# Kernel optimization log

Measured on AMD Instinct MI355X. Metric: run time of the kernel, lower is better.

## Reference

```python
import jax, jax.numpy as jnp
import numpy as np
import math

N = 100000      # nodes
E = 1600000     # edges
D = 128         # in_channels
C = 256         # number of dominant-set cliques
HID = 64        # mlp_hidden
RATIO = 0.8
K = int(math.ceil(RATIO * N))  # 80000 topk nodes per view


def setup_inputs() -> dict:
    key = jax.random.key(0)
    ks = jax.random.split(key, 18)
    s = 0.05
    return {
        "x": jax.random.normal(ks[0], (N, D), jnp.float32),
        "edge_index": jax.random.randint(ks[1], (2, E), 0, N, dtype=jnp.int32),
        "batch": jnp.zeros((N,), jnp.int32),
        "cluster_id": jax.random.randint(ks[2], (N,), 0, C, dtype=jnp.int32),
        # MLP scorer: Linear(D,HID) -> ReLU -> Linear(HID,1)
        "mlp_w1": jax.random.normal(ks[3], (D, HID), jnp.float32) * s,
        "mlp_b1": jnp.zeros((HID,), jnp.float32),
        "mlp_w2": jax.random.normal(ks[4], (HID, 1), jnp.float32) * s,
        "mlp_b2": jnp.zeros((1,), jnp.float32),
        # GATConv(D, 1, heads=1)
        "gat_w": jax.random.normal(ks[5], (D, 1), jnp.float32) * s,
        "gat_a_src": jax.random.normal(ks[6], (1,), jnp.float32) * s,
        "gat_a_dst": jax.random.normal(ks[7], (1,), jnp.float32) * s,
        "gat_b": jnp.zeros((1,), jnp.float32),
        # InterChannelGCN attention Linear(2D,1) split into fine/coarse halves
        "att_w_fine": jax.random.normal(ks[8], (D,), jnp.float32) * s,
        "att_w_coarse": jax.random.normal(ks[9], (D,), jnp.float32) * s,
        "att_b": jnp.zeros((1,), jnp.float32),
        # InterChannelGCN transform Linear(D,D)
        "trans_w": jax.random.normal(ks[10], (D, D), jnp.float32) * s,
        "trans_b": jnp.zeros((D,), jnp.float32),
    }


def _inter_channel_gcn(h_fine, H_coarse, R, wa, wb, ab, tw, tb):
    # attention(Linear(2D,1)) on concat(h_fine_i, H_coarse_j) == h_fine@wa + H_coarse@wb + b
    scores = h_fine @ wa[:, None] + (H_coarse @ wb)[None, :] + ab[0]   # [K, C]
    attn = jax.nn.softmax(scores * R, axis=-1)                          # mask-by-multiply, as original
    out = attn @ H_coarse + h_fine                                      # add_self=True
    return jax.nn.relu(out @ tw + tb)                                   # normalize=False


def reference(x, edge_index, batch, cluster_id,
              mlp_w1, mlp_b1, mlp_w2, mlp_b2,
              gat_w, gat_a_src, gat_a_dst, gat_b,
              att_w_fine, att_w_coarse, att_b, trans_w, trans_b):
    src, dst = edge_index[0], edge_index[1]

    # --- DominantClustering('avg'): cluster means as coarse features ---
    counts = jax.ops.segment_sum(jnp.ones((N,), jnp.float32), cluster_id, num_segments=C)
    Hcoarse = jax.ops.segment_sum(x, cluster_id, num_segments=C) / jnp.maximum(counts, 1.0)[:, None]

    # --- feature view: MLP score + topk ---
    feature_score = (jax.nn.relu(x @ mlp_w1 + mlp_b1) @ mlp_w2 + mlp_b2)[:, 0]   # [N]
    _, feat_idx = jax.lax.top_k(feature_score, K)
    feature_view3 = x[feat_idx]
    R_feat = jax.nn.one_hot(cluster_id[feat_idx], C, dtype=x.dtype)              # relationship matrix
    fuse1 = _inter_channel_gcn(feature_view3, Hcoarse, R_feat,
                               att_w_fine, att_w_coarse, att_b, trans_w, trans_b)

    # --- local view: GATConv(D,1,heads=1) score + topk ---
    h = x @ gat_w                                                                 # [N,1]
    e = jax.nn.leaky_relu(gat_a_src[0] * h[src, 0] + gat_a_dst[0] * h[dst, 0], 0.2)  # [E]
    m = jax.ops.segment_max(e, dst, num_segments=N)
    ex = jnp.exp(e - m[dst])
    den = jax.ops.segment_sum(ex, dst, num_segments=N)
    alpha = ex / jnp.maximum(den[dst], 1e-16)
    localview_score = jax.ops.segment_sum(alpha * h[src, 0], dst, num_segments=N) + gat_b[0]
    _, local_idx = jax.lax.top_k(localview_score, K)
    local_view1 = x[local_idx]
    R_local = jax.nn.one_hot(cluster_id[local_idx], C, dtype=x.dtype)
    fuse2 = _inter_channel_gcn(local_view1, Hcoarse, R_local,
                               att_w_fine, att_w_coarse, att_b, trans_w, trans_b)

    # --- union, edge filtering + remapping (padded fixed shapes) ---
    in_feat = jnp.zeros((N,), bool).at[feat_idx].set(True)
    in_local = jnp.zeros((N,), bool).at[local_idx].set(True)
    union = in_feat | in_local
    mapping = jnp.where(union, jnp.cumsum(union.astype(jnp.int32)) - 1, -1)
    m0, m1 = mapping[src], mapping[dst]
    valid = (m0 >= 0) & (m1 >= 0)
    edge_index_topk = jnp.where(valid[None, :], jnp.stack([m0, m1]), -1)          # [2,E], -1 = dropped

    # --- fused features (faithful to original's fuse1/fuse2 index swap) ---
    A = jnp.zeros((N, D), x.dtype).at[feat_idx].set(fuse2)    # fuse2 indexed by feature topk position
    B = jnp.zeros((N, D), x.dtype).at[local_idx].set(fuse1)   # fuse1 indexed by local topk position
    both = in_feat & in_local
    Fp = jnp.where(both[:, None], (A + B) * 0.5, A + B)
    Fp = jnp.where(union[:, None], Fp, 0.0)                   # [N,D], zero outside union

    new_batch = jnp.where(union, batch, -1)
    return Fp, edge_index_topk, new_batch
```

## Files before the change

kernel.cpp:

```cpp
#include <hip/hip_runtime.h>
#include <hip/hip_bf16.h>
#include <stdint.h>

#define N 100000
#define E_ 1600000
#define D 128
#define C_ 256
#define HID 64
#define KSEL 80000
#define NB 4096
#define CHUNK 1024
#define NCHUNK ((N + CHUNK - 1) / CHUNK)
#define CSEG 32
#define NBK 782
#define BCAP 2560
#define RMAX 2048

__device__ __forceinline__ unsigned enc_f(float f) {
  unsigned b = __float_as_uint(f);
  return (b & 0x80000000u) ? ~b : (b | 0x80000000u);
}
__device__ __forceinline__ float dec_f(unsigned u) {
  unsigned b = (u & 0x80000000u) ? (u ^ 0x80000000u) : ~u;
  return __uint_as_float(b);
}

__global__ __launch_bounds__(256) void k_hist_cluster(const int* __restrict__ cid, int* __restrict__ ccount) {
  int n = blockIdx.x * 256 + threadIdx.x;
  if (n < N) atomicAdd(&ccount[cid[n]], 1);
}

__global__ __launch_bounds__(1024) void k_scan_small(const int* __restrict__ in0, int* __restrict__ out0, int n) {
  __shared__ int sums[1024];
  const int* in = in0 + (size_t)blockIdx.x * n;
  int* out = out0 + (size_t)blockIdx.x * n;
  int t = threadIdx.x;
  int per = (n + 1023) / 1024;
  int base = t * per;
  int loc = 0;
  for (int k = 0; k < per; ++k) { int i = base + k; if (i < n) loc += in[i]; }
  sums[t] = loc; __syncthreads();
  for (int off = 1; off < 1024; off <<= 1) {
    int v = (t >= off) ? sums[t - off] : 0;
    __syncthreads();
    sums[t] += v;
    __syncthreads();
  }
  int run = (t == 0) ? 0 : sums[t - 1];
  for (int k = 0; k < per; ++k) { int i = base + k; if (i < n) { out[i] = run; run += in[i]; } }
}

__global__ __launch_bounds__(256) void k_scatter_cluster(const int* __restrict__ cid, const int* __restrict__ cstart,
                                                         int* __restrict__ ccur, int* __restrict__ cslot) {
  int n = blockIdx.x * 256 + threadIdx.x;
  if (n < N) {
    int c = cid[n];
    int p = cstart[c] + atomicAdd(&ccur[c], 1);
    cslot[p] = n;
  }
}

__global__ __launch_bounds__(128) void k_cluster_partial(const float* __restrict__ x, const int* __restrict__ cstart,
                                                         const int* __restrict__ ccount, const int* __restrict__ cslot,
                                                         float* __restrict__ Hc) {
  int c = blockIdx.x >> 5;
  int s = blockIdx.x & (CSEG - 1);
  int d = threadIdx.x;
  int st = cstart[c], cnt = ccount[c];
  int seg = (cnt + CSEG - 1) / CSEG;
  int lo = s * seg;
  int hi = min(cnt, lo + seg);
  if (lo >= hi) return;
  float acc = 0.f;
  int k = lo;
  for (; k + 2 <= hi; k += 2) {
    int n0 = cslot[st + k], n1 = cslot[st + k + 1];
    float v0 = x[(size_t)n0 * D + d];
    float v1 = x[(size_t)n1 * D + d];
    acc += v0 + v1;
  }
  if (k < hi) acc += x[(size_t)cslot[st + k] * D + d];
  atomicAdd(&Hc[(size_t)c * D + d], acc);
}

__global__ __launch_bounds__(128) void k_mean_gdot(const int* __restrict__ ccount, const float* __restrict__ wb,
                                                   float* __restrict__ Hc, float* __restrict__ gdot) {
  __shared__ float red[128];
  int c = blockIdx.x, d = threadIdx.x;
  float hv = Hc[(size_t)c * D + d] / (float)max(ccount[c], 1);
  Hc[(size_t)c * D + d] = hv;
  red[d] = hv * wb[d];
  __syncthreads();
  if (d < 64) {
    float v = red[d] + red[d + 64];
    for (int off = 32; off; off >>= 1) v += __shfl_down(v, off);
    if (d == 0) gdot[c] = v;
  }
}

__global__ __launch_bounds__(128) void k_S_SW_HW(const float* __restrict__ Hc, const float* __restrict__ tw,
                                                 float* __restrict__ SW, float* __restrict__ HW) {
  __shared__ float Sl[128];
  int b = blockIdx.x, t = threadIdx.x;
  if (b == 0) {
    float s = 0.f;
    for (int c = 0; c < C_; ++c) s += Hc[(size_t)c * D + t];
    Sl[t] = s;
    __syncthreads();
    float acc = 0.f;
    for (int d = 0; d < D; ++d) acc = fmaf(Sl[d], tw[(size_t)d * D + t], acc);
    SW[t] = acc;
  } else {
    const float* src = Hc + (size_t)(b - 1) * D;
    float acc = 0.f;
    for (int d = 0; d < D; ++d) acc = fmaf(src[d], tw[(size_t)d * D + t], acc);
    HW[(size_t)(b - 1) * D + t] = acc;
  }
}

__global__ __launch_bounds__(256, 4) void k_score64(const float* __restrict__ x, const float* __restrict__ w1,
                                                    const float* __restrict__ b1, const float* __restrict__ w2,
                                                    const float* __restrict__ b2, const float* __restrict__ gw,
                                                    const float* __restrict__ wa, float* __restrict__ scoreF,
                                                    float* __restrict__ hg, float* __restrict__ aDot) {
  __shared__ float xld[64 * D];
  int tid = threadIdx.x;
  int base = blockIdx.x * 64;
#pragma unroll
  for (int k = 0; k < 8; ++k) {
    int i = k * 256 + tid;
    int r = i >> 5, off = i & 31;
    int n = base + r;
    float4 v = make_float4(0.f, 0.f, 0.f, 0.f);
    if (n < N) v = ((const float4*)(x + (size_t)n * D))[off];
    ((float4*)xld)[i] = v;
  }
  __syncthreads();

  int rg = tid >> 5;
  int cg = tid & 31;
  int c2 = cg * 2;
  float acc[8][2] = {};
  const float* xb = xld + rg * 8 * D;
  for (int d4 = 0; d4 < D; d4 += 4) {
    float2 wv0 = *(const float2*)(w1 + (size_t)(d4 + 0) * HID + c2);
    float2 wv1 = *(const float2*)(w1 + (size_t)(d4 + 1) * HID + c2);
    float2 wv2 = *(const float2*)(w1 + (size_t)(d4 + 2) * HID + c2);
    float2 wv3 = *(const float2*)(w1 + (size_t)(d4 + 3) * HID + c2);
#pragma unroll
    for (int r = 0; r < 8; ++r) {
      float4 xv = *(const float4*)(xb + r * D + d4);
      acc[r][0] = fmaf(xv.x, wv0.x, acc[r][0]);
      acc[r][1] = fmaf(xv.x, wv0.y, acc[r][1]);
      acc[r][0] = fmaf(xv.y, wv1.x, acc[r][0]);
      acc[r][1] = fmaf(xv.y, wv1.y, acc[r][1]);
      acc[r][0] = fmaf(xv.z, wv2.x, acc[r][0]);
      acc[r][1] = fmaf(xv.z, wv2.y, acc[r][1]);
      acc[r][0] = fmaf(xv.w, wv3.x, acc[r][0]);
      acc[r][1] = fmaf(xv.w, wv3.y, acc[r][1]);
    }
  }
  float2 b1v = *(const float2*)(b1 + c2);
  float2 w2v = *(const float2*)(w2 + c2);
  float bb = b2[0];
#pragma unroll
  for (int r = 0; r < 8; ++r) {
    float p = fmaxf(acc[r][0] + b1v.x, 0.f) * w2v.x + fmaxf(acc[r][1] + b1v.y, 0.f) * w2v.y;
#pragma unroll
    for (int off = 16; off; off >>= 1) p += __shfl_xor(p, off);
    if (cg == 0) {
      int n = base + rg * 8 + r;
      if (n < N) scoreF[n] = p + bb;
    }
  }
  float4 gwv = *(const float4*)(gw + cg * 4);
  float4 wav = *(const float4*)(wa + cg * 4);
#pragma unroll
  for (int r = 0; r < 8; ++r) {
    int row = rg * 8 + r;
    float4 xv = *(const float4*)(xld + row * D + cg * 4);
    float hp = xv.x * gwv.x + xv.y * gwv.y + xv.z * gwv.z + xv.w * gwv.w;
    float ap = xv.x * wav.x + xv.y * wav.y + xv.z * wav.z + xv.w * wav.w;
#pragma unroll
    for (int off = 16; off; off >>= 1) {
      hp += __shfl_xor(hp, off);
      ap += __shfl_xor(ap, off);
    }
    if (cg == 0) {
      int n = base + row;
      if (n < N) { hg[n] = hp; aDot[n] = ap; }
    }
  }
}

__global__ __launch_bounds__(1024) void k_escatter(const int* __restrict__ ei, const float* __restrict__ hg,
                                                   const float* __restrict__ asrc, const float* __restrict__ adst,
                                                   int* __restrict__ gcnt, uint2* __restrict__ payload) {
  __shared__ int lcnt[NBK];
  __shared__ int lbase[NBK];
  int tid = threadIdx.x;
  for (int i = tid; i < NBK; i += 1024) lcnt[i] = 0;
  int e0 = blockIdx.x * 8192;
  int es[8], ed[8];
#pragma unroll
  for (int k = 0; k < 8; ++k) {
    int e = e0 + k * 1024 + tid;
    bool v = (e < E_);
    es[k] = v ? ei[e] : -1;
    ed[k] = v ? ei[E_ + e] : -1;
  }
  __syncthreads();
#pragma unroll
  for (int k = 0; k < 8; ++k)
    if (ed[k] >= 0) atomicAdd(&lcnt[ed[k] >> 7], 1);
  __syncthreads();
  for (int i = tid; i < NBK; i += 1024) {
    int c = lcnt[i];
    lbase[i] = c ? atomicAdd(&gcnt[i], c) : 0;
    lcnt[i] = 0;
  }
  __syncthreads();
  float as = asrc[0], ad = adst[0];
#pragma unroll
  for (int k = 0; k < 8; ++k) {
    if (ed[k] < 0) continue;
    int s = es[k], d = ed[k];
    int b = d >> 7, dl = d & 127;
    float z = as * hg[s] + ad * hg[d];
    float ev = (z > 0.f) ? z : 0.2f * z;
    int pos = lbase[b] + atomicAdd(&lcnt[b], 1);
    if (pos < BCAP) {
      uint2 rec;
      rec.x = __float_as_uint(ev);
      rec.y = (unsigned)s | ((unsigned)dl << 24);
      payload[(size_t)b * BCAP + pos] = rec;
    }
  }
}

__global__ __launch_bounds__(256) void k_esoftmax(const uint2* __restrict__ payload, const int* __restrict__ gcnt,
                                                  const float* __restrict__ hg, const float* __restrict__ gb,
                                                  float* __restrict__ scoreL) {
  __shared__ unsigned mS[128];
  __shared__ float dS[128];
  __shared__ float nS[128];
  int b = blockIdx.x;
  int tid = threadIdx.x;
  if (tid < 128) { mS[tid] = 0u; dS[tid] = 0.f; nS[tid] = 0.f; }
  __syncthreads();
  int cnt = min(gcnt[b], BCAP);
  const uint2* bp = payload + (size_t)b * BCAP;
  for (int i = tid; i < cnt; i += 256) {
    uint2 r = bp[i];
    atomicMax(&mS[r.y >> 24], enc_f(__uint_as_float(r.x)));
  }
  __syncthreads();
  for (int i = tid; i < cnt; i += 256) {
    uint2 r = bp[i];
    int d = r.y >> 24;
    float ex = expf(__uint_as_float(r.x) - dec_f(mS[d]));
    atomicAdd(&dS[d], ex);
  }
  __syncthreads();
  for (int i = tid; i < cnt; i += 256) {
    uint2 r = bp[i];
    int d = r.y >> 24;
    float ex = expf(__uint_as_float(r.x) - dec_f(mS[d]));
    float alpha = ex / fmaxf(dS[d], 1e-16f);
    float h = hg[r.y & 0xFFFFFFu];
    atomicAdd(&nS[d], alpha * h);
  }
  __syncthreads();
  if (tid < 128) {
    int dst = b * 128 + tid;
    if (dst < N) scoreL[dst] = nS[tid] + gb[0];
  }
}

__global__ __launch_bounds__(256) void k_minmax2(const float* __restrict__ sc2, unsigned* __restrict__ mm) {
  __shared__ unsigned smx[256], smn[256];
  int v = blockIdx.y;
  const float* sc = sc2 + (size_t)v * N;
  int t = threadIdx.x; int n = blockIdx.x * 256 + t;
  unsigned val = (n < N) ? enc_f(sc[n]) : 0u;
  smx[t] = (n < N) ? val : 0u;
  smn[t] = (n < N) ? val : 0xFFFFFFFFu;
  __syncthreads();
  for (int off = 128; off; off >>= 1) {
    if (t < off) {
      smx[t] = max(smx[t], smx[t + off]);
      smn[t] = min(smn[t], smn[t + off]);
    }
    __syncthreads();
  }
  if (t == 0) { atomicMax(&mm[v], smx[0]); atomicMin(&mm[2 + v], smn[0]); }
}

__global__ __launch_bounds__(256) void k_bucket_hist2(const float* __restrict__ sc2, const unsigned* __restrict__ mm,
                                                      int* __restrict__ bucket2, int* __restrict__ hist2) {
  int v = blockIdx.y;
  int n = blockIdx.x * 256 + threadIdx.x;
  if (n >= N) return;
  const float* sc = sc2 + (size_t)v * N;
  float smax = dec_f(mm[v]), smin = dec_f(mm[2 + v]);
  float range = smax - smin;
  float scale = (range > 0.f) ? ((float)NB / range) : 0.f;
  float t = (smax - sc[n]) * scale;
  int b = (int)t;
  b = b < 0 ? 0 : (b > NB - 1 ? NB - 1 : b);
  bucket2[(size_t)v * N + n] = b;
  atomicAdd(&hist2[v * NB + b], 1);
}

__global__ __launch_bounds__(256) void k_bucket_scatter2(const int* __restrict__ bucket2, const int* __restrict__ start2,
                                                         int* __restrict__ cur2, int* __restrict__ slot2) {
  int v = blockIdx.y;
  int n = blockIdx.x * 256 + threadIdx.x;
  if (n >= N) return;
  int b = bucket2[(size_t)v * N + n];
  slot2[(size_t)v * N + start2[v * NB + b] + atomicAdd(&cur2[v * NB + b], 1)] = n;
}

__global__ __launch_bounds__(64) void k_bucket_rank3(const float* __restrict__ sc2, const int* __restrict__ start2,
                                                     const int* __restrict__ hist2, const int* __restrict__ slot2,
                                                     int* __restrict__ rank2, int* __restrict__ sorted2) {
  __shared__ unsigned long long keys[RMAX];
  int v = blockIdx.y;
  int b = blockIdx.x;
  int st = start2[v * NB + b], cnt = hist2[v * NB + b];
  if (cnt == 0) return;
  const float* sc = sc2 + (size_t)v * N;
  const int* slot = slot2 + (size_t)v * N;
  int* rank = rank2 + (size_t)v * N;
  int* sorted = sorted2 + (size_t)v * N;
  int tid = threadIdx.x;
  if (cnt <= RMAX) {
    for (int i = tid; i < cnt; i += 64) {
      int m = slot[st + i];
      keys[i] = (((unsigned long long)(~enc_f(sc[m]))) << 32) | (unsigned)m;
    }
    __syncthreads();
    for (int i = tid; i < cnt; i += 64) {
      unsigned long long mykey = keys[i];
      int r = 0;
      for (int j = 0; j < cnt; ++j) r += (keys[j] < mykey) ? 1 : 0;
      int m = (int)(mykey & 0xFFFFFFFFu);
      rank[m] = st + r;
      sorted[st + r] = m;
    }
  } else {
    for (int i = tid; i < cnt; i += 64) {
      int m = slot[st + i];
      unsigned long long mykey = (((unsigned long long)(~enc_f(sc[m]))) << 32) | (unsigned)m;
      int r = 0;
      for (int j = 0; j < cnt; ++j) {
        int mj = slot[st + j];
        unsigned long long k = (((unsigned long long)(~enc_f(sc[mj]))) << 32) | (unsigned)mj;
        r += (k < mykey) ? 1 : 0;
      }
      rank[m] = st + r;
      sorted[st + r] = m;
    }
  }
}

__global__ __launch_bounds__(1024) void k_union_chunksum(const int* __restrict__ rankF, const int* __restrict__ rankL,
                                                         int* __restrict__ csum) {
  __shared__ int red[1024];
  int t = threadIdx.x; int i = blockIdx.x * 1024 + t;
  int u = (i < N) ? (((rankF[i] < KSEL) || (rankL[i] < KSEL)) ? 1 : 0) : 0;
  red[t] = u; __syncthreads();
  for (int off = 512; off; off >>= 1) { if (t < off) red[t] += red[t + off]; __syncthreads(); }
  if (t == 0) csum[blockIdx.x] = red[0];
}

__global__ __launch_bounds__(1024) void k_union_map(const int* __restrict__ rankF, const int* __restrict__ rankL,
                                                    const int* __restrict__ cstart, const int* __restrict__ batch,
                                                    int* __restrict__ mapping, float* __restrict__ outBatch) {
  __shared__ int sums[1024];
  int t = threadIdx.x; int i = blockIdx.x * 1024 + t;
  int u = (i < N) ? (((rankF[i] < KSEL) || (rankL[i] < KSEL)) ? 1 : 0) : 0;
  sums[t] = u; __syncthreads();
  for (int off = 1; off < 1024; off <<= 1) {
    int v = (t >= off) ? sums[t - off] : 0;
    __syncthreads();
    sums[t] += v;
    __syncthreads();
  }
  if (i < N) {
    mapping[i] = u ? (cstart[blockIdx.x] + sums[t] - 1) : -1;
    outBatch[i] = u ? (float)batch[i] : -1.0f;
  }
}

__global__ __launch_bounds__(256) void k_edge_out(const int* __restrict__ ei, const int* __restrict__ mapping,
                                                  float* __restrict__ outE) {
  int e = blockIdx.x * 256 + threadIdx.x;
  if (e >= E_) return;
  int m0 = mapping[ei[e]], m1 = mapping[ei[E_ + e]];
  bool valid = (m0 >= 0) && (m1 >= 0);
  outE[e] = valid ? (float)m0 : -1.f;
  outE[E_ + e] = valid ? (float)m1 : -1.f;
}

__global__ __launch_bounds__(256) void k_zero_rows(const int* __restrict__ mapping, float* __restrict__ Fp) {
  int i = blockIdx.x * 256 + threadIdx.x;
  int n = i >> 5;
  if (n < N && mapping[n] < 0) ((float4*)Fp)[i] = make_float4(0.f, 0.f, 0.f, 0.f);
}

__global__ __launch_bounds__(256, 4) void k_fuse64(const float* __restrict__ x, const float* __restrict__ tw,
                                                   const float* __restrict__ tb, const float* __restrict__ SW,
                                                   const float* __restrict__ HW, const float* __restrict__ gdot,
                                                   const float* __restrict__ aDot, const int* __restrict__ cid,
                                                   const int* __restrict__ srcL, const int* __restrict__ tgtL,
                                                   const float* __restrict__ attb, const int* __restrict__ rankF,
                                                   float* __restrict__ Fp, int accum) {
  __shared__ float xld[64 * D];
  __shared__ float pq[64 * 2];
  __shared__ int mt[64 * 2];
  __shared__ int ft[64];
  int tid = threadIdx.x;
  int base = blockIdx.x * 64;
  if (tid < 64) {
    int ws = srcL[base + tid];
    int cc = cid[ws];
    int tg = tgtL[base + tid];
    mt[tid * 2] = cc;
    mt[tid * 2 + 1] = tg;
    ft[tid] = (rankF[tg] < KSEL) ? 1 : 0;
    float s = aDot[ws] + gdot[cc] + attb[0];
    float mx = fmaxf(s, 0.f);
    float esm = expf(s - mx), eom = expf(-mx);
    float dn = esm + 255.f * eom;
    pq[tid * 2] = esm / dn;
    pq[tid * 2 + 1] = eom / dn;
  }
#pragma unroll
  for (int k = 0; k < 8; ++k) {
    int i = k * 256 + tid;
    int r = i >> 5, off = i & 31;
    int ws = srcL[base + r];
    ((float4*)xld)[i] = ((const float4*)(x + (size_t)ws * D))[off];
  }
  __syncthreads();

  int rg = tid >> 5;
  int c4 = (tid & 31) * 4;
  float acc[8][4] = {};
  const float* xb = xld + rg * 8 * D;
  float4 t0 = *(const float4*)(tw + (size_t)0 * D + c4);
  float4 t1 = *(const float4*)(tw + (size_t)1 * D + c4);
  float4 t2 = *(const float4*)(tw + (size_t)2 * D + c4);
  float4 t3 = *(const float4*)(tw + (size_t)3 * D + c4);
  for (int d4 = 0; d4 < D; d4 += 4) {
    float4 u0, u1, u2, u3;
    if (d4 + 4 < D) {
      u0 = *(const float4*)(tw + (size_t)(d4 + 4) * D + c4);
      u1 = *(const float4*)(tw + (size_t)(d4 + 5) * D + c4);
      u2 = *(const float4*)(tw + (size_t)(d4 + 6) * D + c4);
      u3 = *(const float4*)(tw + (size_t)(d4 + 7) * D + c4);
    } else {
      u0 = u1 = u2 = u3 = make_float4(0.f, 0.f, 0.f, 0.f);
    }
#pragma unroll
    for (int r = 0; r < 8; ++r) {
      float4 xv = *(const float4*)(xb + r * D + d4);
      acc[r][0] = fmaf(xv.x, t0.x, acc[r][0]);
      acc[r][1] = fmaf(xv.x, t0.y, acc[r][1]);
      acc[r][2] = fmaf(xv.x, t0.z, acc[r][2]);
      acc[r][3] = fmaf(xv.x, t0.w, acc[r][3]);
      acc[r][0] = fmaf(xv.y, t1.x, acc[r][0]);
      acc[r][1] = fmaf(xv.y, t1.y, acc[r][1]);
      acc[r][2] = fmaf(xv.y, t1.z, acc[r][2]);
      acc[r][3] = fmaf(xv.y, t1.w, acc[r][3]);
      acc[r][0] = fmaf(xv.z, t2.x, acc[r][0]);
      acc[r][1] = fmaf(xv.z, t2.y, acc[r][1]);
      acc[r][2] = fmaf(xv.z, t2.z, acc[r][2]);
      acc[r][3] = fmaf(xv.z, t2.w, acc[r][3]);
      acc[r][0] = fmaf(xv.w, t3.x, acc[r][0]);
      acc[r][1] = fmaf(xv.w, t3.y, acc[r][1]);
      acc[r][2] = fmaf(xv.w, t3.z, acc[r][2]);
      acc[r][3] = fmaf(xv.w, t3.w, acc[r][3]);
    }
    t0 = u0; t1 = u1; t2 = u2; t3 = u3;
  }

  float4 tbv = *(const float4*)(tb + c4);
  float4 swv = *(const float4*)(SW + c4);
#pragma unroll
  for (int r = 0; r < 8; ++r) {
    int row = rg * 8 + r;
    float p = pq[row * 2], q = pq[row * 2 + 1];
    int cc = mt[row * 2];
    int tgt = mt[row * 2 + 1];
    float4 hw = *(const float4*)(HW + (size_t)cc * D + c4);
    float4 o;
    o.x = fmaxf(acc[r][0] + tbv.x + q * swv.x + (p - q) * hw.x, 0.f);
    o.y = fmaxf(acc[r][1] + tbv.y + q * swv.y + (p - q) * hw.y, 0.f);
    o.z = fmaxf(acc[r][2] + tbv.z + q * swv.z + (p - q) * hw.z, 0.f);
    o.w = fmaxf(acc[r][3] + tbv.w + q * swv.w + (p - q) * hw.w, 0.f);
    float4* dst = (float4*)(Fp + (size_t)tgt * D + c4);
    if (accum && ft[row]) {
      float4 old = *dst;
      o.x = (o.x + old.x) * 0.5f;
      o.y = (o.y + old.y) * 0.5f;
      o.z = (o.z + old.z) * 0.5f;
      o.w = (o.w + old.w) * 0.5f;
    }
    *dst = o;
  }
}

extern "C" void kernel_launch(void* const* d_in, const int* in_sizes, int n_in,
                              void* d_out, int out_size, void* d_ws, size_t ws_size,
                              hipStream_t stream) {
  const float* x   = (const float*)d_in[0];
  const int* ei    = (const int*)d_in[1];
  const int* batch = (const int*)d_in[2];
  const int* cid   = (const int*)d_in[3];
  const float* w1  = (const float*)d_in[4];
  const float* b1  = (const float*)d_in[5];
  const float* w2  = (const float*)d_in[6];
  const float* b2  = (const float*)d_in[7];
  const float* gw  = (const float*)d_in[8];
  const float* gas = (const float*)d_in[9];
  const float* gad = (const float*)d_in[10];
  const float* gb  = (const float*)d_in[11];
  const float* wa  = (const float*)d_in[12];
  const float* wb  = (const float*)d_in[13];
  const float* ab  = (const float*)d_in[14];
  const float* tw  = (const float*)d_in[15];
  const float* tb  = (const float*)d_in[16];
  (void)in_sizes; (void)n_in; (void)ws_size; (void)out_size;

  char* p = (char*)d_ws;
  auto alloc = [&](size_t bytes) -> char* {
    char* r = p;
    p += (bytes + 255) & ~(size_t)255;
    return r;
  };
  int* ccount    = (int*)alloc(C_ * 4);
  int* ccur      = (int*)alloc(C_ * 4);
  unsigned* mm   = (unsigned*)alloc(16);
  int* hist2     = (int*)alloc(2 * NB * 4);
  int* cur2      = (int*)alloc(2 * NB * 4);
  float* Hc      = (float*)alloc((size_t)C_ * D * 4);
  int* gcnt      = (int*)alloc(NBK * 4);
  size_t zeroBytes = (size_t)(p - (char*)d_ws);
  int* cstart   = (int*)alloc(C_ * 4);
  int* cslot    = (int*)alloc((size_t)N * 4);
  float* gdot   = (float*)alloc(C_ * 4);
  float* SW     = (float*)alloc(D * 4);
  float* HW     = (float*)alloc((size_t)C_ * D * 4);
  float* score2 = (float*)alloc((size_t)2 * N * 4);
  float* hg     = (float*)alloc((size_t)N * 4);
  float* aDot   = (float*)alloc((size_t)N * 4);
  uint2* payload = (uint2*)alloc((size_t)NBK * BCAP * 8);
  int* bucket2  = (int*)alloc((size_t)2 * N * 4);
  int* start2   = (int*)alloc(2 * NB * 4);
  int* slot2    = (int*)alloc((size_t)2 * N * 4);
  int* sorted2  = (int*)alloc((size_t)2 * N * 4);
  int* rank2    = (int*)alloc((size_t)2 * N * 4);
  int* csums    = (int*)alloc(NCHUNK * 4);
  int* cstarts  = (int*)alloc(NCHUNK * 4);
  int* mapping  = (int*)alloc((size_t)N * 4);

  float* scoreF = score2;
  float* scoreL = score2 + N;
  int* sortedF  = sorted2;
  int* sortedL  = sorted2 + N;
  int* rankF    = rank2;
  int* rankL    = rank2 + N;

  float* outF = (float*)d_out;
  float* outE = outF + (size_t)N * D;
  float* outB = outE + (size_t)2 * E_;

  hipMemsetAsync(d_ws, 0, zeroBytes, stream);
  hipMemsetAsync(mm + 2, 0xFF, 8, stream);

  k_hist_cluster<<<(N + 255) / 256, 256, 0, stream>>>(cid, ccount);
  k_scan_small<<<1, 1024, 0, stream>>>(ccount, cstart, C_);
  k_scatter_cluster<<<(N + 255) / 256, 256, 0, stream>>>(cid, cstart, ccur, cslot);
  k_cluster_partial<<<C_ * CSEG, 128, 0, stream>>>(x, cstart, ccount, cslot, Hc);
  k_mean_gdot<<<C_, 128, 0, stream>>>(ccount, wb, Hc, gdot);
  k_S_SW_HW<<<C_ + 1, 128, 0, stream>>>(Hc, tw, SW, HW);

  k_score64<<<(N + 63) / 64, 256, 0, stream>>>(x, w1, b1, w2, b2, gw, wa, scoreF, hg, aDot);
  k_escatter<<<(E_ + 8191) / 8192, 1024, 0, stream>>>(ei, hg, gas, gad, gcnt, payload);
  k_esoftmax<<<NBK, 256, 0, stream>>>(payload, gcnt, hg, gb, scoreL);

  dim3 g2((N + 255) / 256, 2);
  k_minmax2<<<g2, 256, 0, stream>>>(score2, mm);
  k_bucket_hist2<<<g2, 256, 0, stream>>>(score2, mm, bucket2, hist2);
  k_scan_small<<<2, 1024, 0, stream>>>(hist2, start2, NB);
  k_bucket_scatter2<<<g2, 256, 0, stream>>>(bucket2, start2, cur2, slot2);
  dim3 gr(NB, 2);
  k_bucket_rank3<<<gr, 64, 0, stream>>>(score2, start2, hist2, slot2, rank2, sorted2);

  k_union_chunksum<<<NCHUNK, 1024, 0, stream>>>(rankF, rankL, csums);
  k_scan_small<<<1, 1024, 0, stream>>>(csums, cstarts, NCHUNK);
  k_union_map<<<NCHUNK, 1024, 0, stream>>>(rankF, rankL, cstarts, batch, mapping, outB);
  k_edge_out<<<(E_ + 255) / 256, 256, 0, stream>>>(ei, mapping, outE);
  k_zero_rows<<<(N * 32 + 255) / 256, 256, 0, stream>>>(mapping, outF);

  k_fuse64<<<KSEL / 64, 256, 0, stream>>>(x, tw, tb, SW, HW, gdot, aDot, cid, sortedL, sortedF, ab, rankF, outF, 0);
  k_fuse64<<<KSEL / 64, 256, 0, stream>>>(x, tw, tb, SW, HW, gdot, aDot, cid, sortedF, sortedL, ab, rankF, outF, 1);
}
```

Measured before the change: 577.3 us.

## Use bf16 MFMA for the fuse-stage transform GEMM

The per-row 128x128 transform inside k_fuse64 moves from scalar fp32 FMAs to bf16 MFMA 16x16x32 instructions. Gathered x rows are converted to bf16 and stored in a swizzled shared buffer of half the size. A new small kernel writes a transposed bf16 copy of the transform weights. This cuts ALU work and LDS footprint in the fuse kernels, at the cost of bf16 rounding error in the output.

```diff
diff --git a/kernel.cpp b/kernel.cpp
--- a/kernel.cpp
+++ b/kernel.cpp
@@ -16,6 +16,9 @@
 #define BCAP 2560
 #define RMAX 2048
 
+typedef __attribute__((ext_vector_type(8))) short bf16x8;
+typedef __attribute__((ext_vector_type(4))) float f32x4;
+
 __device__ __forceinline__ unsigned enc_f(float f) {
   unsigned b = __float_as_uint(f);
   return (b & 0x80000000u) ? ~b : (b | 0x80000000u);
@@ -23,6 +26,12 @@
 __device__ __forceinline__ float dec_f(unsigned u) {
   unsigned b = (u & 0x80000000u) ? (u ^ 0x80000000u) : ~u;
   return __uint_as_float(b);
+}
+
+__device__ __forceinline__ unsigned short f2bf(float f) {
+  unsigned u = __float_as_uint(f);
+  unsigned r = u + 0x7FFFu + ((u >> 16) & 1u);
+  return (unsigned short)(r >> 16);
 }
 
 __global__ __launch_bounds__(256) void k_hist_cluster(const int* __restrict__ cid, int* __restrict__ ccount) {
@@ -118,6 +127,12 @@
   }
 }
 
+__global__ __launch_bounds__(128) void k_twT(const float* __restrict__ tw, unsigned short* __restrict__ twT) {
+  int k = blockIdx.x;
+  int o = threadIdx.x;
+  twT[(size_t)o * D + k] = f2bf(tw[(size_t)k * D + o]);
+}
+
 __global__ __launch_bounds__(256, 4) void k_score64(const float* __restrict__ x, const float* __restrict__ w1,
                                                     const float* __restrict__ b1, const float* __restrict__ w2,
                                                     const float* __restrict__ b2, const float* __restrict__ gw,
@@ -409,14 +424,14 @@
   if (n < N && mapping[n] < 0) ((float4*)Fp)[i] = make_float4(0.f, 0.f, 0.f, 0.f);
 }
 
-__global__ __launch_bounds__(256, 4) void k_fuse64(const float* __restrict__ x, const float* __restrict__ tw,
+__global__ __launch_bounds__(256, 4) void k_fuse64(const float* __restrict__ x, const unsigned short* __restrict__ twT,
                                                    const float* __restrict__ tb, const float* __restrict__ SW,
                                                    const float* __restrict__ HW, const float* __restrict__ gdot,
                                                    const float* __restrict__ aDot, const int* __restrict__ cid,
                                                    const int* __restrict__ srcL, const int* __restrict__ tgtL,
                                                    const float* __restrict__ attb, const int* __restrict__ rankF,
                                                    float* __restrict__ Fp, int accum) {
-  __shared__ float xld[64 * D];
+  __shared__ __align__(16) unsigned xw[64 * 64];
   __shared__ float pq[64 * 2];
   __shared__ int mt[64 * 2];
   __shared__ int ft[64];
@@ -439,69 +454,53 @@
 #pragma unroll
   for (int k = 0; k < 8; ++k) {
     int i = k * 256 + tid;
-    int r = i >> 5, off = i & 31;
+    int r = i >> 5, c4 = i & 31;
     int ws = srcL[base + r];
-    ((float4*)xld)[i] = ((const float4*)(x + (size_t)ws * D))[off];
-  }
-  __syncthreads();
-
-  int rg = tid >> 5;
-  int c4 = (tid & 31) * 4;
-  float acc[8][4] = {};
-  const float* xb = xld + rg * 8 * D;
-  float4 t0 = *(const float4*)(tw + (size_t)0 * D + c4);
-  float4 t1 = *(const float4*)(tw + (size_t)1 * D + c4);
-  float4 t2 = *(const float4*)(tw + (size_t)2 * D + c4);
-  float4 t3 = *(const float4*)(tw + (size_t)3 * D + c4);
-  for (int d4 = 0; d4 < D; d4 += 4) {
-    float4 u0, u1, u2, u3;
-    if (d4 + 4 < D) {
-      u0 = *(const float4*)(tw + (size_t)(d4 + 4) * D + c4);
-      u1 = *(const float4*)(tw + (size_t)(d4 + 5) * D + c4);
-      u2 = *(const float4*)(tw + (size_t)(d4 + 6) * D + c4);
-      u3 = *(const float4*)(tw + (size_t)(d4 + 7) * D + c4);
-    } else {
-      u0 = u1 = u2 = u3 = make_float4(0.f, 0.f, 0.f, 0.f);
-    }
-#pragma unroll
-    for (int r = 0; r < 8; ++r) {
-      float4 xv = *(const float4*)(xb + r * D + d4);
-      acc[r][0] = fmaf(xv.x, t0.x, acc[r][0]);
-      acc[r][1] = fmaf(xv.x, t0.y, acc[r][1]);
-      acc[r][2] = fmaf(xv.x, t0.z, acc[r][2]);
-      acc[r][3] = fmaf(xv.x, t0.w, acc[r][3]);
-      acc[r][0] = fmaf(xv.y, t1.x, acc[r][0]);
-      acc[r][1] = fmaf(xv.y, t1.y, acc[r][1]);
-      acc[r][2] = fmaf(xv.y, t1.z, acc[r][2]);
-      acc[r][3] = fmaf(xv.y, t1.w, acc[r][3]);
-      acc[r][0] = fmaf(xv.z, t2.x, acc[r][0]);
-      acc[r][1] = fmaf(xv.z, t2.y, acc[r][1]);
-      acc[r][2] = fmaf(xv.z, t2.z, acc[r][2]);
-      acc[r][3] = fmaf(xv.z, t2.w, acc[r][3]);
-      acc[r][0] = fmaf(xv.w, t3.x, acc[r][0]);
-      acc[r][1] = fmaf(xv.w, t3.y, acc[r][1]);
-      acc[r][2] = fmaf(xv.w, t3.z, acc[r][2]);
-      acc[r][3] = fmaf(xv.w, t3.w, acc[r][3]);
-    }
-    t0 = u0; t1 = u1; t2 = u2; t3 = u3;
-  }
-
-  float4 tbv = *(const float4*)(tb + c4);
-  float4 swv = *(const float4*)(SW + c4);
-#pragma unroll
-  for (int r = 0; r < 8; ++r) {
-    int row = rg * 8 + r;
-    float p = pq[row * 2], q = pq[row * 2 + 1];
-    int cc = mt[row * 2];
-    int tgt = mt[row * 2 + 1];
-    float4 hw = *(const float4*)(HW + (size_t)cc * D + c4);
+    float4 v = ((const float4*)(x + (size_t)ws * D))[c4];
+    uint2 pk;
+    pk.x = (unsigned)f2bf(v.x) | ((unsigned)f2bf(v.y) << 16);
+    pk.y = (unsigned)f2bf(v.z) | ((unsigned)f2bf(v.w) << 16);
+    int u2 = r * 32 + (c4 ^ ((r & 7) << 1));
+    ((uint2*)xw)[u2] = pk;
+  }
+  __syncthreads();
+
+  int w = tid >> 6;
+  int l = tid & 63;
+  int nl = l & 15;
+  int khalf = l >> 4;
+  int row = w * 16 + nl;
+
+  f32x4 acc[8] = {};
+  const char* xbase = (const char*)xw + row * 256;
+  unsigned rsw = (unsigned)((row & 7) << 4);
+#pragma unroll
+  for (int ks = 0; ks < 4; ++ks) {
+    bf16x8 bfrag = *(const bf16x8*)(xbase + (((unsigned)(ks * 64 + khalf * 16)) ^ rsw));
+#pragma unroll
+    for (int ot = 0; ot < 8; ++ot) {
+      bf16x8 afrag = *(const bf16x8*)(twT + (size_t)(ot * 16 + nl) * D + ks * 32 + khalf * 8);
+      acc[ot] = __builtin_amdgcn_mfma_f32_16x16x32_bf16(afrag, bfrag, acc[ot], 0, 0, 0);
+    }
+  }
+
+  float p = pq[row * 2], q = pq[row * 2 + 1];
+  int cc = mt[row * 2];
+  int tgt = mt[row * 2 + 1];
+  int doAcc = accum && ft[row];
+#pragma unroll
+  for (int ot = 0; ot < 8; ++ot) {
+    int ch = ot * 16 + khalf * 4;
+    float4 tbv = *(const float4*)(tb + ch);
+    float4 swv = *(const float4*)(SW + ch);
+    float4 hw = *(const float4*)(HW + (size_t)cc * D + ch);
     float4 o;
-    o.x = fmaxf(acc[r][0] + tbv.x + q * swv.x + (p - q) * hw.x, 0.f);
-    o.y = fmaxf(acc[r][1] + tbv.y + q * swv.y + (p - q) * hw.y, 0.f);
-    o.z = fmaxf(acc[r][2] + tbv.z + q * swv.z + (p - q) * hw.z, 0.f);
-    o.w = fmaxf(acc[r][3] + tbv.w + q * swv.w + (p - q) * hw.w, 0.f);
-    float4* dst = (float4*)(Fp + (size_t)tgt * D + c4);
-    if (accum && ft[row]) {
+    o.x = fmaxf(acc[ot][0] + tbv.x + q * swv.x + (p - q) * hw.x, 0.f);
+    o.y = fmaxf(acc[ot][1] + tbv.y + q * swv.y + (p - q) * hw.y, 0.f);
+    o.z = fmaxf(acc[ot][2] + tbv.z + q * swv.z + (p - q) * hw.z, 0.f);
+    o.w = fmaxf(acc[ot][3] + tbv.w + q * swv.w + (p - q) * hw.w, 0.f);
+    float4* dst = (float4*)(Fp + (size_t)tgt * D + ch);
+    if (doAcc) {
       float4 old = *dst;
       o.x = (o.x + old.x) * 0.5f;
       o.y = (o.y + old.y) * 0.5f;
@@ -553,6 +552,7 @@
   float* gdot   = (float*)alloc(C_ * 4);
   float* SW     = (float*)alloc(D * 4);
   float* HW     = (float*)alloc((size_t)C_ * D * 4);
+  unsigned short* twT = (unsigned short*)alloc((size_t)D * D * 2);
   float* score2 = (float*)alloc((size_t)2 * N * 4);
   float* hg     = (float*)alloc((size_t)N * 4);
   float* aDot   = (float*)alloc((size_t)N * 4);
@@ -586,6 +586,7 @@
   k_cluster_partial<<<C_ * CSEG, 128, 0, stream>>>(x, cstart, ccount, cslot, Hc);
   k_mean_gdot<<<C_, 128, 0, stream>>>(ccount, wb, Hc, gdot);
   k_S_SW_HW<<<C_ + 1, 128, 0, stream>>>(Hc, tw, SW, HW);
+  k_twT<<<D, D, 0, stream>>>(tw, twT);
 
   k_score64<<<(N + 63) / 64, 256, 0, stream>>>(x, w1, b1, w2, b2, gw, wa, scoreF, hg, aDot);
   k_escatter<<<(E_ + 8191) / 8192, 1024, 0, stream>>>(ei, hg, gas, gad, gcnt, payload);
@@ -605,6 +606,6 @@
   k_edge_out<<<(E_ + 255) / 256, 256, 0, stream>>>(ei, mapping, outE);
   k_zero_rows<<<(N * 32 + 255) / 256, 256, 0, stream>>>(mapping, outF);
 
-  k_fuse64<<<KSEL / 64, 256, 0, stream>>>(x, tw, tb, SW, HW, gdot, aDot, cid, sortedL, sortedF, ab, rankF, outF, 0);
-  k_fuse64<<<KSEL / 64, 256, 0, stream>>>(x, tw, tb, SW, HW, gdot, aDot, cid, sortedF, sortedL, ab, rankF, outF, 1);
-}
+  k_fuse64<<<KSEL / 64, 256, 0, stream>>>(x, twT, tb, SW, HW, gdot, aDot, cid, sortedL, sortedF, ab, rankF, outF, 0);
+  k_fuse64<<<KSEL / 64, 256, 0, stream>>>(x, twT, tb, SW, HW, gdot, aDot, cid, sortedF, sortedL, ab, rankF, outF, 1);
+}
```

Result: faster. 559.4 us (-3.1%).
